# Performance work log

Measured on AMD Instinct MI355X. Metric: run time of the kernel, lower is better.

Reference implementation:

```python
import jax, jax.numpy as jnp
import numpy as np

EPS = 1e-12  # VERY_SMALL_NUMBER
LN_EPS = 1e-5
N, NFEAT, NHID, A, P, HOPS = 50000, 256, 128, 32, 4, 2


def setup_inputs() -> dict:
    key = jax.random.key(0)
    ks = jax.random.split(key, 16)
    def w(i, shape, scale=0.05):
        return jax.random.normal(ks[i], shape, dtype=jnp.float32) * scale
    return {
        "x": jax.random.normal(ks[0], (N, NFEAT), dtype=jnp.float32),
        # input_mapper: Linear(nfeat,nhid) -> ReLU -> Linear(nhid,nhid)
        "im_w1": w(1, (NFEAT, NHID)), "im_b1": jnp.zeros((NHID,), jnp.float32),
        "im_w2": w(2, (NHID, NHID)),  "im_b2": jnp.zeros((NHID,), jnp.float32),
        # AnchorGraphLearner
        "anchors": w(3, (A, NHID), 1.0),
        "ml_w1": w(4, (P, 2 * NHID, NHID)), "ml_b1": jnp.zeros((P, NHID), jnp.float32),
        "ml_w2": w(5, (P, NHID)),            "ml_b2": jnp.zeros((P,), jnp.float32),
        # AnchorGNNLayer weights (xavier in torch; scaled randn here)
        "enc_w": w(6, (HOPS, NHID, NHID)), "enc_b": jnp.zeros((HOPS, NHID), jnp.float32),
        # LayerNorm
        "ln_g": jnp.ones((NHID,), jnp.float32), "ln_b": jnp.zeros((NHID,), jnp.float32),
        # classifier: Linear -> PReLU(nhid) -> Linear(nhid,2)
        "cls_w1": w(7, (NHID, NHID)), "cls_b1": jnp.zeros((NHID,), jnp.float32),
        "prelu_a": jnp.full((NHID,), 0.25, jnp.float32),
        "cls_w2": w(8, (NHID, 2)),   "cls_b2": jnp.zeros((2,), jnp.float32),
    }


def _forward(x, im_w1, im_b1, im_w2, im_b2, anchors, ml_w1, ml_b1, ml_w2, ml_b2,
             enc_w, enc_b, ln_g, ln_b, cls_w1, cls_b1, prelu_a, cls_w2, cls_b2):
    nhid = im_w2.shape[-1]
    # input_mapper (dropout is identity in eval)
    h = jnp.maximum(x @ im_w1 + im_b1, 0.0) @ im_w2 + im_b2  # [N, nhid]
    x_loc = h

    # --- AnchorGraphLearner: fused form of cat([x_i, a_j]) @ W1 ---
    Wx, Wa = ml_w1[:, :nhid, :], ml_w1[:, nhid:, :]  # each [P, nhid, nhid]
    attn = jnp.zeros((h.shape[0], anchors.shape[0]), h.dtype)
    for p in range(ml_w1.shape[0]):  # small fixed head count
        hx = h @ Wx[p]                               # [N, nhid]
        ha = anchors @ Wa[p]                         # [A, nhid]
        hid = jnp.maximum(hx[:, None, :] + ha[None, :, :] + ml_b1[p], 0.0)  # [N, A, nhid]
        attn = attn + jax.nn.sigmoid(hid @ ml_w2[p] + ml_b2[p])            # [N, A]
    adj = attn / ml_w1.shape[0]  # mean over heads, [N, A]

    # --- AnchorGNNLayer stack (anchor_mp normalized double matmul) ---
    node_norm = adj / jnp.maximum(adj.sum(axis=0, keepdims=True), EPS)     # col-normalized [N, A]
    anchor_norm = adj / jnp.maximum(adj.sum(axis=1, keepdims=True), EPS)   # row-normalized [N, A]
    xc = h
    for i in range(enc_w.shape[0]):
        support = xc @ enc_w[i]                          # [N, nhid]
        agg = node_norm.T @ support                      # [A, nhid]
        xc = jnp.maximum(anchor_norm @ agg + enc_b[i], 0.0)

    # residual + LayerNorm
    z = xc + x_loc
    mu = z.mean(axis=-1, keepdims=True)
    var = ((z - mu) ** 2).mean(axis=-1, keepdims=True)
    z = (z - mu) * jax.lax.rsqrt(var + LN_EPS) * ln_g + ln_b

    def classifier(t):
        t1 = t @ cls_w1 + cls_b1
        t1 = jnp.where(t1 > 0, t1, prelu_a * t1)  # PReLU(nhid)
        return t1 @ cls_w2 + cls_b2

    pred = classifier(z)                 # [N, 2]
    anchor_logits = classifier(anchors)  # [A, 2]
    anchor_vec = anchors[None]           # [1, A, nhid] (matches unsqueeze(0))
    return (pred, z, anchor_vec, anchor_logits)


def reference(x, im_w1, im_b1, im_w2, im_b2, anchors, ml_w1, ml_b1, ml_w2, ml_b2,
              enc_w, enc_b, ln_g, ln_b, cls_w1, cls_b1, prelu_a, cls_w2, cls_b2):
    return _forward(x, im_w1, im_b1, im_w2, im_b2, anchors, ml_w1, ml_b1, ml_w2, ml_b2,
                    enc_w, enc_b, ln_g, ln_b, cls_w1, cls_b1, prelu_a, cls_w2, cls_b2)
```

## Files before the change

### kernel.cpp

```cpp
#include <hip/hip_runtime.h>
#include <math.h>

#define NN 50000
#define FEAT 256
#define HID 128
#define NA 32
#define NP 4
#define TM 64
#define NBLK 782
#define NB2 781
#define LDA 132
#define EPSS 1e-12f
#define LN_EPS 1e-5f

typedef unsigned short u16;
typedef __attribute__((ext_vector_type(8))) short bf16x8;
typedef __attribute__((ext_vector_type(4))) float f32x4;

#define ADJ_F   0
#define RS_F    1600000
#define CS_F    1650000
#define AGG0_F  1650032
#define AGG1_F  1654128
#define HB_F    1658256
#define FLAG_F  1674640
#define F_END   1674672
#define XC_U   (2 * F_END)
#define SUP_U  (XC_U + NN * HID)
#define PW_U   (SUP_U + NN * HID)
#define PW_TOT 165638
#define WS_NEED_BYTES ((size_t)(PW_U + PW_TOT) * 2ULL)
#define CSP_OFF 0

#define PK_IMW1T  0
#define PK_IMW2T  32768
#define PK_MLW1T  49152
#define PK_ENCWT  114688
#define PK_CLSW1T 147456
#define PK_IMB1   163840
#define PK_IMB2   163968
#define PK_MLW2   164096
#define PK_ENCB   164608
#define PK_LNG    164864
#define PK_LNB    164992
#define PK_CLSB1  165120
#define PK_PRELU  165248
#define PK_CLSW2  165376
#define PK_CLSB2  165632
#define PK_MLB2   165634
#define PK_TOTAL  165638

#define PRED_OFF 0
#define Z_OFF    100000
#define AV_OFF   6500000
#define AL_OFF   6504096
#define OUT_TOT  6504160

__device__ __constant__ int kNel[19] = {
    NN * FEAT, FEAT * HID, HID, HID * HID, HID, NA * HID,
    NP * 2 * HID * HID, NP * HID, NP * HID, NP, 2 * HID * HID, 2 * HID,
    HID, HID, HID * HID, HID, HID, HID * 2, 2};

#define TSEG_TOT 163840
__device__ __constant__ int tLen[9]  = {32768,16384,16384,16384,16384,16384,16384,16384,16384};
__device__ __constant__ int tDst[9]  = {PK_IMW1T,PK_IMW2T,PK_MLW1T,PK_MLW1T+16384,
                                        PK_MLW1T+32768,PK_MLW1T+49152,PK_ENCWT,
                                        PK_ENCWT+16384,PK_CLSW1T};
__device__ __constant__ int tSrcT[9] = {1,3,6,6,6,6,10,10,14};
__device__ __constant__ int tBase[9] = {0,0,0,32768,65536,98304,0,16384,0};
#define VSEG_TOT 1798
__device__ __constant__ int vLen[11] = {128,128,512,256,128,128,128,128,256,2,4};
__device__ __constant__ int vDst[11] = {PK_IMB1,PK_IMB2,PK_MLW2,PK_ENCB,PK_LNG,PK_LNB,
                                        PK_CLSB1,PK_PRELU,PK_CLSW2,PK_CLSB2,PK_MLB2};
__device__ __constant__ int vSrcT[11]= {2,4,8,11,12,13,15,16,17,18,9};

struct P19 { const void* q[19]; };

__device__ __forceinline__ float b2f(u16 u) {
    union { float f; unsigned int i; } v; v.i = ((unsigned int)u) << 16; return v.f;
}
__device__ __forceinline__ u16 f2b(float f) {
    union { float f; unsigned int i; } v; v.f = f;
    unsigned int x = v.i;
    x += 0x7fffu + ((x >> 16) & 1u);
    return (u16)(x >> 16);
}
__device__ __forceinline__ float ldf(const void* p, size_t i, int fl) {
    if (fl == 1) return ((const float*)p)[i];
    if (fl == 0) return b2f(((const u16*)p)[i]);
    return 0.f;
}

__global__ __launch_bounds__(256) void k_detect_all(P19 a, int* __restrict__ flags) {
    __shared__ int sHi[256], sE[256], sO[256];
    const int b = blockIdx.x;
    const u16* p = (const u16*)a.q[b];
    const int M = (kNel[b] < 8192) ? kNel[b] : 8192;
    int cHi = 0, cE = 0, cO = 0;
    for (int j = threadIdx.x; j < M; j += 256) {
        const u16 v = p[j];
        if (j & 1) cO += (v != 0);
        else { cE += (v != 0); cHi += (((v >> 7) & 0xFF) >= 200); }
    }
    sHi[threadIdx.x] = cHi; sE[threadIdx.x] = cE; sO[threadIdx.x] = cO;
    __syncthreads();
    for (int s = 128; s > 0; s >>= 1) {
        if (threadIdx.x < (unsigned)s) {
            sHi[threadIdx.x] += sHi[threadIdx.x + s];
            sE[threadIdx.x]  += sE[threadIdx.x + s];
            sO[threadIdx.x]  += sO[threadIdx.x + s];
        }
        __syncthreads();
    }
    if (threadIdx.x == 0) {
        int f;
        if (sE[0] == 0 && sO[0] == 0) f = 2;
        else if (sHi[0] >= 4 || sE[0] == 0) f = 1;
        else f = 0;
        flags[b] = f;
    }
}

__global__ __launch_bounds__(256) void k_convT(P19 a, const int* __restrict__ flags,
                                               u16* __restrict__ pw) {
    int idx = blockIdx.x * 256 + threadIdx.x;
    if (idx >= TSEG_TOT) return;
    int off = idx, s = 0;
    while (off >= tLen[s]) { off -= tLen[s]; ++s; }
    int n, k;
    if (s == 0) { n = off >> 8; k = off & 255; }
    else        { n = off >> 7; k = off & 127; }
    const int si = tSrcT[s];
    pw[tDst[s] + off] = f2b(ldf(a.q[si], (size_t)tBase[s] + (size_t)k * 128 + n,
                                flags[si]));
}

__global__ __launch_bounds__(256) void k_convV(P19 a, const int* __restrict__ flags,
                                               u16* __restrict__ pw) {
    for (int idx = threadIdx.x; idx < VSEG_TOT; idx += 256) {
        int off = idx, s = 0;
        while (off >= vLen[s]) { off -= vLen[s]; ++s; }
        const int si = vSrcT[s];
        pw[vDst[s] + off] = f2b(ldf(a.q[si], off, flags[si]));
    }
}

__device__ __forceinline__ void mfma_64x128(const u16* As, const u16* Bt,
                                            f32x4 acc[8], int lane, int rowBase) {
    const int lr = lane & 15, lq = lane >> 4;
#pragma unroll
    for (int kc = 0; kc < 4; ++kc) {
        bf16x8 a = *(const bf16x8*)(As + (rowBase + lr) * 136 + kc * 32 + lq * 8);
#pragma unroll
        for (int t = 0; t < 8; ++t) {
            bf16x8 b = *(const bf16x8*)(Bt + (t * 16 + lr) * 136 + kc * 32 + lq * 8);
            acc[t] = __builtin_amdgcn_mfma_f32_16x16x32_bf16(a, b, acc[t], 0, 0, 0);
        }
    }
}

template<int KTOT, int ACT, int AMODE, int OMODE>
__global__ __launch_bounds__(256) void k_gemm_m(const void* __restrict__ A,
                                                const u16* __restrict__ pw,
                                                void* __restrict__ outp,
                                                const int* __restrict__ flags,
                                                const int boff, const int biasOff) {
    __shared__ __align__(16) u16 As[64 * 136];
    __shared__ __align__(16) u16 Bt[128 * 136];
    const int fA = (AMODE == 0) ? flags[0] : 0;
    const int tid = threadIdx.x;
    const int row0 = blockIdx.x * TM;
    const int lane = tid & 63, wv = tid >> 6, rowBase = wv * 16;
    const int lr = lane & 15, lq = lane >> 4;
    f32x4 acc[8];
    const f32x4 z4 = {0.f, 0.f, 0.f, 0.f};
#pragma unroll
    for (int t = 0; t < 8; ++t) acc[t] = z4;

    for (int kc = 0; kc < KTOT / 128; ++kc) {
        for (int i = tid; i < 64 * 32; i += 256) {
            const int m = i >> 5, k4 = (i & 31) << 2;
            const int g = row0 + m;
            ushort4 o; o.x = 0; o.y = 0; o.z = 0; o.w = 0;
            if (g < NN) {
                const size_t idx = (size_t)g * KTOT + kc * 128 + k4;
                bool f32path = (AMODE == 2) || (AMODE == 0 && fA == 1);
                if (f32path) {
                    float4 v = *(const float4*)((const float*)A + idx);
                    o.x = f2b(v.x); o.y = f2b(v.y); o.z = f2b(v.z); o.w = f2b(v.w);
                } else {
                    o = *(const ushort4*)((const u16*)A + idx);
                }
            }
            *(ushort4*)&As[m * 136 + k4] = o;
        }
        for (int i = tid; i < 128 * 32; i += 256) {
            const int n = i >> 5, k4 = (i & 31) << 2;
            *(ushort4*)&Bt[n * 136 + k4] =
                *(const ushort4*)(pw + boff + (size_t)n * KTOT + kc * 128 + k4);
        }
        __syncthreads();
        mfma_64x128(As, Bt, acc, lane, rowBase);
        __syncthreads();
    }
#pragma unroll
    for (int t = 0; t < 8; ++t) {
        const int col = t * 16 + lr;
        const float bv = (biasOff >= 0) ? b2f(pw[biasOff + col]) : 0.f;
#pragma unroll
        for (int r = 0; r < 4; ++r) {
            const int g = row0 + rowBase + lq * 4 + r;
            if (g < NN) {
                float v = acc[t][r] + bv;
                if (ACT == 1) v = fmaxf(v, 0.f);
                if constexpr (OMODE == 0)
                    ((u16*)outp)[(size_t)g * HID + col] = f2b(v);
                else
                    ((float*)outp)[(size_t)g * HID + col] = v;
            }
        }
    }
}

__global__ __launch_bounds__(128) void k_pre(const void* __restrict__ anchors,
                                             const void* __restrict__ ml_w1,
                                             const void* __restrict__ ml_b1,
                                             float* __restrict__ hb,
                                             const int* __restrict__ flags) {
    __shared__ float sa[HID];
    const int fAn = flags[5], fW1 = flags[6], fB1 = flags[7];
    const int p = blockIdx.x >> 5, a = blockIdx.x & 31, k = threadIdx.x;
    sa[k] = ldf(anchors, a * HID + k, fAn);
    __syncthreads();
    float acc = ldf(ml_b1, p * HID + k, fB1);
    const size_t wbase = ((size_t)p * 2 * HID + HID) * HID + k;
#pragma unroll 4
    for (int j = 0; j < HID; ++j)
        acc += sa[j] * ldf(ml_w1, wbase + (size_t)j * HID, fW1);
    hb[p * (NA * HID) + k * NA + a] = acc;
}

__global__ __launch_bounds__(128) void k_wc(const float* __restrict__ hb,
                                            const u16* __restrict__ pw,
                                            float* __restrict__ wc) {
    __shared__ float red[128];
    const int p = blockIdx.x, tid = threadIdx.x;
    const int a = tid & 31, q = tid >> 5;
    float s = 0.f;
    for (int k = q * 32; k < q * 32 + 32; ++k)
        s += b2f(pw[PK_MLW2 + p * HID + k]) * hb[(size_t)p * (NA * HID) + k * NA + a];
    red[tid] = 0.5f * s;
    __syncthreads();
    if (tid < 32)
        wc[p * NA + tid] = red[tid] + red[tid + 32] + red[tid + 64] + red[tid + 96];
}

__global__ __launch_bounds__(256) void k_anchor(const void* __restrict__ anchors,
                                                const void* __restrict__ cls_w1,
                                                const void* __restrict__ cls_b1,
                                                const void* __restrict__ prelu_a,
                                                const void* __restrict__ cls_w2,
                                                const void* __restrict__ cls_b2,
                                                float* __restrict__ out,
                                                const int* __restrict__ flags) {
    __shared__ float sa[2][HID];
    __shared__ float st1[2][HID];
    const int fAn = flags[5], fW1 = flags[14], fB1 = flags[15];
    const int fPa = flags[16], fW2 = flags[17], fB2 = flags[18];
    const int tid = threadIdx.x;
    const int a0 = blockIdx.x * 2;
    const int half = tid >> 7, k = tid & 127;
    sa[half][k] = ldf(anchors, (a0 + half) * HID + k, fAn);
    __syncthreads();
    float acc = ldf(cls_b1, k, fB1);
#pragma unroll 4
    for (int j = 0; j < HID; ++j) acc += sa[half][j] * ldf(cls_w1, j * HID + k, fW1);
    const float pa = ldf(prelu_a, k, fPa);
    st1[half][k] = acc > 0.f ? acc : pa * acc;
    __syncthreads();
    if (tid < 4) {
        const int aa = tid >> 1, c = tid & 1;
        float s = ldf(cls_b2, c, fB2);
        for (int j = 0; j < HID; ++j) s += st1[aa][j] * ldf(cls_w2, j * 2 + c, fW2);
        out[AL_OFF + (a0 + aa) * 2 + c] = s;
    }
    if (blockIdx.x == 0) {
        for (int i = tid; i < NA * HID; i += 256)
            out[AV_OFF + i] = ldf(anchors, i, fAn);
    }
}

__global__ __launch_bounds__(256) void k_fattn(const float* __restrict__ h,
                                               const u16* __restrict__ pw,
                                               const float* __restrict__ hb,
                                               const float* __restrict__ wc,
                                               float* __restrict__ adj,
                                               float* __restrict__ rowsum,
                                               float* __restrict__ csPart) {
    __shared__ __align__(16) u16 Bt[128 * 136];
    __shared__ __align__(16) float hbs[128 * 32];
    __shared__ float hws[HID];
    __shared__ float wcs[NA];
    __shared__ float swr[4][NA];
    const int tid = threadIdx.x;
    const int row0 = blockIdx.x * TM;
    const int lane = tid & 63, wv = tid >> 6, rowBase = wv * 16;
    const int lr = lane & 15, lq = lane >> 4;
    const int g = tid & 3, myrow = tid >> 2;
    const int a0 = g * 8;

    bf16x8 afr[4];
    {
        const int gr = row0 + rowBase + lr;
#pragma unroll
        for (int kc = 0; kc < 4; ++kc) {
            bf16x8 t;
            if (gr < NN) {
                const float* src = h + (size_t)gr * HID + kc * 32 + lq * 8;
                float4 v0 = *(const float4*)src;
                float4 v1 = *(const float4*)(src + 4);
                t[0] = (short)f2b(v0.x); t[1] = (short)f2b(v0.y);
                t[2] = (short)f2b(v0.z); t[3] = (short)f2b(v0.w);
                t[4] = (short)f2b(v1.x); t[5] = (short)f2b(v1.y);
                t[6] = (short)f2b(v1.z); t[7] = (short)f2b(v1.w);
            } else {
#pragma unroll
                for (int j = 0; j < 8; ++j) t[j] = 0;
            }
            afr[kc] = t;
        }
    }

    float adjacc[8];
#pragma unroll
    for (int j = 0; j < 8; ++j) adjacc[j] = 0.f;

    for (int p = 0; p < NP; ++p) {
        __syncthreads();
        for (int i = tid; i < 128 * 32; i += 256) {
            const int n = i >> 5, k4 = (i & 31) << 2;
            *(ushort4*)&Bt[n * 136 + k4] =
                *(const ushort4*)(pw + PK_MLW1T + p * 16384 + n * 128 + k4);
        }
        const float* hbp = hb + (size_t)p * (NA * HID);
        for (int i = tid; i < 1024; i += 256)
            *(float4*)&hbs[i * 4] = *(const float4*)(hbp + i * 4);
        if (tid < HID) hws[tid] = 0.5f * b2f(pw[PK_MLW2 + p * HID + tid]);
        if (tid < NA) wcs[tid] = wc[p * NA + tid];
        __syncthreads();

        f32x4 acc[8];
        const f32x4 z4 = {0.f, 0.f, 0.f, 0.f};
#pragma unroll
        for (int t = 0; t < 8; ++t) acc[t] = z4;
#pragma unroll
        for (int kc = 0; kc < 4; ++kc)
#pragma unroll
            for (int t = 0; t < 8; ++t) {
                bf16x8 b = *(const bf16x8*)(Bt + (t * 16 + lr) * 136 + kc * 32 + lq * 8);
                acc[t] = __builtin_amdgcn_mfma_f32_16x16x32_bf16(afr[kc], b, acc[t], 0, 0, 0);
            }
        __syncthreads();
#pragma unroll
        for (int t = 0; t < 8; ++t)
#pragma unroll
            for (int r = 0; r < 4; ++r)
                Bt[(rowBase + lq * 4 + r) * 136 + t * 16 + lr] = f2b(acc[t][r]);
        __syncthreads();

        const float b2v = b2f(pw[PK_MLB2 + p]);
        float sabs[8], wh = 0.f;
#pragma unroll
        for (int j = 0; j < 8; ++j) sabs[j] = 0.f;

#pragma unroll 4
        for (int kp = 0; kp < 64; ++kp) {
            const unsigned hx2 = *(const unsigned*)&Bt[myrow * 136 + kp * 2];
            union { unsigned u; float f; } u0, u1;
            u0.u = hx2 << 16;
            u1.u = hx2 & 0xffff0000u;
            const float f0 = u0.f, f1 = u1.f;
            const float2 hw2 = *(const float2*)&hws[kp * 2];
            wh = fmaf(hw2.x, f0, wh);
            wh = fmaf(hw2.y, f1, wh);
            const float4 c00 = *(const float4*)&hbs[(kp * 2) * NA + a0];
            const float4 c01 = *(const float4*)&hbs[(kp * 2) * NA + a0 + 4];
            const float4 c10 = *(const float4*)&hbs[(kp * 2 + 1) * NA + a0];
            const float4 c11 = *(const float4*)&hbs[(kp * 2 + 1) * NA + a0 + 4];
            sabs[0] = fmaf(hw2.x, fabsf(f0 + c00.x), sabs[0]);
            sabs[1] = fmaf(hw2.x, fabsf(f0 + c00.y), sabs[1]);
            sabs[2] = fmaf(hw2.x, fabsf(f0 + c00.z), sabs[2]);
            sabs[3] = fmaf(hw2.x, fabsf(f0 + c00.w), sabs[3]);
            sabs[4] = fmaf(hw2.x, fabsf(f0 + c01.x), sabs[4]);
            sabs[5] = fmaf(hw2.x, fabsf(f0 + c01.y), sabs[5]);
            sabs[6] = fmaf(hw2.x, fabsf(f0 + c01.z), sabs[6]);
            sabs[7] = fmaf(hw2.x, fabsf(f0 + c01.w), sabs[7]);
            sabs[0] = fmaf(hw2.y, fabsf(f1 + c10.x), sabs[0]);
            sabs[1] = fmaf(hw2.y, fabsf(f1 + c10.y), sabs[1]);
            sabs[2] = fmaf(hw2.y, fabsf(f1 + c10.z), sabs[2]);
            sabs[3] = fmaf(hw2.y, fabsf(f1 + c10.w), sabs[3]);
            sabs[4] = fmaf(hw2.y, fabsf(f1 + c11.x), sabs[4]);
            sabs[5] = fmaf(hw2.y, fabsf(f1 + c11.y), sabs[5]);
            sabs[6] = fmaf(hw2.y, fabsf(f1 + c11.z), sabs[6]);
            sabs[7] = fmaf(hw2.y, fabsf(f1 + c11.w), sabs[7]);
        }
#pragma unroll
        for (int j = 0; j < 8; ++j) {
            const float s = wh + wcs[a0 + j] + b2v + sabs[j];
            adjacc[j] += 0.25f / (1.f + __expf(-s));
        }
    }

    const int grow = row0 + myrow;
    if (grow >= NN) {
#pragma unroll
        for (int j = 0; j < 8; ++j) adjacc[j] = 0.f;
    }
    if (grow < NN) {
        float* dst = adj + (size_t)grow * NA + a0;
        *(float4*)dst = make_float4(adjacc[0], adjacc[1], adjacc[2], adjacc[3]);
        *(float4*)(dst + 4) = make_float4(adjacc[4], adjacc[5], adjacc[6], adjacc[7]);
    }
    float rs = 0.f;
#pragma unroll
    for (int j = 0; j < 8; ++j) rs += adjacc[j];
    rs += __shfl_xor(rs, 1);
    rs += __shfl_xor(rs, 2);
    if (g == 0 && grow < NN) rowsum[grow] = rs;
#pragma unroll
    for (int st = 4; st <= 32; st <<= 1)
#pragma unroll
        for (int j = 0; j < 8; ++j) adjacc[j] += __shfl_xor(adjacc[j], st);
    if (lane < 4) {
#pragma unroll
        for (int j = 0; j < 8; ++j) swr[wv][lane * 8 + j] = adjacc[j];
    }
    __syncthreads();
    if (tid < NA)
        csPart[tid * NBLK + blockIdx.x] =
            swr[0][tid] + swr[1][tid] + swr[2][tid] + swr[3][tid];
}

__global__ __launch_bounds__(256) void k_cs_red(const float* __restrict__ csPart,
                                                float* __restrict__ colsum) {
    __shared__ float red[256];
    const int a = blockIdx.x, tid = threadIdx.x;
    float s = 0.f;
    for (int b = tid; b < NBLK; b += 256) s += csPart[a * NBLK + b];
    red[tid] = s;
    __syncthreads();
    for (int st = 128; st > 0; st >>= 1) {
        if (tid < st) red[tid] += red[tid + st];
        __syncthreads();
    }
    if (tid == 0) colsum[a] = red[0];
}

__global__ __launch_bounds__(256) void k_aggT(const float* __restrict__ adj,
                                              const float* __restrict__ h,
                                              float* __restrict__ part) {
    __shared__ float sT[TM][LDA];
    __shared__ float adjT[TM][NA + 1];
    const int tid = threadIdx.x;
    const int a0 = (tid & 15) * 2, k0 = (tid >> 4) * 8;
    float acc[2][8];
#pragma unroll
    for (int ia = 0; ia < 2; ++ia)
#pragma unroll
        for (int j = 0; j < 8; ++j) acc[ia][j] = 0.f;

    const int nt = (blockIdx.x == NB2 - 1) ? 2 : 1;
    for (int t = 0; t < nt; ++t) {
        const int row0 = (blockIdx.x + t) * TM;
        __syncthreads();
        for (int i = tid; i < TM * 32; i += 256) {
            const int m = i >> 5, k4 = (i & 31) << 2, g = row0 + m;
            float4 v = make_float4(0.f, 0.f, 0.f, 0.f);
            if (g < NN) v = *(const float4*)(h + (size_t)g * HID + k4);
            *(float4*)&sT[m][k4] = v;
        }
        for (int i = tid; i < TM * NA; i += 256) {
            const int m = i >> 5, a = i & 31, g = row0 + m;
            adjT[m][a] = (g < NN) ? adj[(size_t)g * NA + a] : 0.f;
        }
        __syncthreads();
#pragma unroll 4
        for (int n = 0; n < TM; ++n) {
            const float a0v = adjT[n][a0], a1v = adjT[n][a0 + 1];
            float4 s0 = *(const float4*)&sT[n][k0];
            float4 s1 = *(const float4*)&sT[n][k0 + 4];
            float sv[8] = {s0.x, s0.y, s0.z, s0.w, s1.x, s1.y, s1.z, s1.w};
#pragma unroll
            for (int j = 0; j < 8; ++j) {
                acc[0][j] += a0v * sv[j];
                acc[1][j] += a1v * sv[j];
            }
        }
    }
    float* dst = part + (size_t)blockIdx.x * (NA * HID);
#pragma unroll
    for (int ia = 0; ia < 2; ++ia) {
        *(float4*)&dst[(a0 + ia) * HID + k0] =
            make_float4(acc[ia][0], acc[ia][1], acc[ia][2], acc[ia][3]);
        *(float4*)&dst[(a0 + ia) * HID + k0 + 4] =
            make_float4(acc[ia][4], acc[ia][5], acc[ia][6], acc[ia][7]);
    }
}

__global__ __launch_bounds__(256) void k_Tred(const float* __restrict__ part,
                                              float* __restrict__ T) {
    __shared__ float red[256];
    const int jj = threadIdx.x & 15, bq = threadIdx.x >> 4;
    const int j = blockIdx.x * 16 + jj;
    float s = 0.f;
#pragma unroll 8
    for (int b = bq; b < NB2; b += 16) s += part[(size_t)b * (NA * HID) + j];
    red[threadIdx.x] = s;
    __syncthreads();
    if (bq == 0) {
        float t = 0.f;
#pragma unroll
        for (int q = 0; q < 16; ++q) t += red[q * 16 + jj];
        T[j] = t;
    }
}

__global__ __launch_bounds__(128) void k_small(const float* __restrict__ T,
                                               const u16* __restrict__ pw,
                                               const int hop,
                                               float* __restrict__ agg) {
    __shared__ float tr[HID];
    const int a = blockIdx.x, n = threadIdx.x;
    tr[n] = T[a * HID + n];
    __syncthreads();
    const u16* w = pw + PK_ENCWT + hop * HID * HID + n * HID;
    float s = 0.f;
#pragma unroll 4
    for (int j4 = 0; j4 < HID; j4 += 4) {
        ushort4 u = *(const ushort4*)(w + j4);
        s += tr[j4] * b2f(u.x) + tr[j4 + 1] * b2f(u.y) +
             tr[j4 + 2] * b2f(u.z) + tr[j4 + 3] * b2f(u.w);
    }
    agg[a * HID + n] = s;
}

__global__ __launch_bounds__(256) void k_e2a(const float* __restrict__ adj,
                                             const float* __restrict__ rowsum,
                                             const float* __restrict__ colsum,
                                             const float* __restrict__ agg,
                                             const u16* __restrict__ pw,
                                             float* __restrict__ part) {
    __shared__ float aggn[NA][LDA];
    __shared__ float adjT[TM][NA + 1];
    __shared__ __align__(8) u16 xcs[TM * 136];
    __shared__ float csl[NA], rsl[TM];
    const int tid = threadIdx.x;
    const int n0 = (tid & 31) * 4, m0 = (tid >> 5) * 8;
    const int a0 = (tid & 15) * 2, k0 = (tid >> 4) * 8;

    if (tid < NA) csl[tid] = fmaxf(colsum[tid], EPSS);
    __syncthreads();
    for (int i = tid; i < (NA * HID) / 4; i += 256) {
        const int a = i >> 5, k4 = (i & 31) << 2;
        float4 v = *(const float4*)(agg + a * HID + k4);
        const float inv = 1.f / csl[a];
        v.x *= inv; v.y *= inv; v.z *= inv; v.w *= inv;
        *(float4*)&aggn[a][k4] = v;
    }
    float bv[4];
#pragma unroll
    for (int j = 0; j < 4; ++j) bv[j] = b2f(pw[PK_ENCB + n0 + j]);

    float acc2[2][8];
#pragma unroll
    for (int ia = 0; ia < 2; ++ia)
#pragma unroll
        for (int j = 0; j < 8; ++j) acc2[ia][j] = 0.f;

    const int nt = (blockIdx.x == NB2 - 1) ? 2 : 1;
    for (int t = 0; t < nt; ++t) {
        const int row0 = (blockIdx.x + t) * TM;
        __syncthreads();
        for (int i = tid; i < TM * NA; i += 256) {
            const int m = i >> 5, a = i & 31, g = row0 + m;
            adjT[m][a] = (g < NN) ? adj[(size_t)g * NA + a] : 0.f;
        }
        if (tid >= 64 && tid < 128) {
            const int m = tid - 64, g = row0 + m;
            rsl[m] = (g < NN) ? 1.f / fmaxf(rowsum[g], EPSS) : 0.f;
        }
        __syncthreads();
        float acc[8][4];
#pragma unroll
        for (int i = 0; i < 8; ++i)
#pragma unroll
            for (int j = 0; j < 4; ++j) acc[i][j] = 0.f;
        for (int a = 0; a < NA; ++a) {
            float4 gv = *(const float4*)&aggn[a][n0];
            float gvv[4] = {gv.x, gv.y, gv.z, gv.w};
#pragma unroll
            for (int i = 0; i < 8; ++i) {
                const float av = adjT[m0 + i][a];
#pragma unroll
                for (int j = 0; j < 4; ++j) acc[i][j] += av * gvv[j];
            }
        }
#pragma unroll
        for (int i = 0; i < 8; ++i) {
            const float r = rsl[m0 + i];
            ushort4 o;
            o.x = f2b(fmaxf(r * acc[i][0] + bv[0], 0.f));
            o.y = f2b(fmaxf(r * acc[i][1] + bv[1], 0.f));
            o.z = f2b(fmaxf(r * acc[i][2] + bv[2], 0.f));
            o.w = f2b(fmaxf(r * acc[i][3] + bv[3], 0.f));
            *(ushort4*)&xcs[(m0 + i) * 136 + n0] = o;
        }
        __syncthreads();
#pragma unroll 4
        for (int n = 0; n < TM; ++n) {
            const float a0v = adjT[n][a0], a1v = adjT[n][a0 + 1];
            ushort4 u0 = *(const ushort4*)&xcs[n * 136 + k0];
            ushort4 u1 = *(const ushort4*)&xcs[n * 136 + k0 + 4];
            float sv[8] = {b2f(u0.x), b2f(u0.y), b2f(u0.z), b2f(u0.w),
                           b2f(u1.x), b2f(u1.y), b2f(u1.z), b2f(u1.w)};
#pragma unroll
            for (int j = 0; j < 8; ++j) {
                acc2[0][j] += a0v * sv[j];
                acc2[1][j] += a1v * sv[j];
            }
        }
    }
    float* dst = part + (size_t)blockIdx.x * (NA * HID);
#pragma unroll
    for (int ia = 0; ia < 2; ++ia) {
        *(float4*)&dst[(a0 + ia) * HID + k0] =
            make_float4(acc2[ia][0], acc2[ia][1], acc2[ia][2], acc2[ia][3]);
        *(float4*)&dst[(a0 + ia) * HID + k0 + 4] =
            make_float4(acc2[ia][4], acc2[ia][5], acc2[ia][6], acc2[ia][7]);
    }
}

__global__ __launch_bounds__(256) void k_e2f(const float* __restrict__ adj,
                                             const float* __restrict__ rowsum,
                                             const float* __restrict__ colsum,
                                             const float* __restrict__ agg,
                                             const u16* __restrict__ pw,
                                             float* __restrict__ out) {
    __shared__ __align__(16) u16 As[64 * 136];
    __shared__ __align__(16) u16 uniB[128 * 136];
    __shared__ float smu[TM], sinv[TM], sg[HID], sb[HID], w2s[2 * HID];
    __shared__ float csl[NA], rsl[TM];
    float* aggn  = (float*)As;
    float* adjTf = (float*)uniB;
    float* zT    = (float*)uniB;
    const int tid = threadIdx.x;
    const int row0 = blockIdx.x * TM;
    const int lane = tid & 63, wv = tid >> 6, rowBase = wv * 16;
    const int lr = lane & 15, lq = lane >> 4;
    const int n0 = (tid & 31) * 4, m0 = (tid >> 5) * 8;
    const float* h = out + Z_OFF;

    if (tid < NA) csl[tid] = fmaxf(colsum[tid], EPSS);
    if (tid >= 64 && tid < 128) {
        const int m = tid - 64, g = row0 + m;
        rsl[m] = (g < NN) ? 1.f / fmaxf(rowsum[g], EPSS) : 0.f;
    }
    for (int i = tid; i < TM * NA; i += 256) {
        const int m = i >> 5, a = i & 31, g = row0 + m;
        adjTf[m * (NA + 1) + a] = (g < NN) ? adj[(size_t)g * NA + a] : 0.f;
    }
    __syncthreads();
    for (int i = tid; i < (NA * HID) / 4; i += 256) {
        const int a = i >> 5, k4 = (i & 31) << 2;
        float4 v = *(const float4*)(agg + a * HID + k4);
        const float inv = 1.f / csl[a];
        v.x *= inv; v.y *= inv; v.z *= inv; v.w *= inv;
        *(float4*)&aggn[a * LDA + k4] = v;
    }
    __syncthreads();
    float acc[8][4];
#pragma unroll
    for (int i = 0; i < 8; ++i)
#pragma unroll
        for (int j = 0; j < 4; ++j) acc[i][j] = 0.f;
    for (int a = 0; a < NA; ++a) {
        float4 gv = *(const float4*)&aggn[a * LDA + n0];
        float gvv[4] = {gv.x, gv.y, gv.z, gv.w};
#pragma unroll
        for (int i = 0; i < 8; ++i) {
            const float av = adjTf[(m0 + i) * (NA + 1) + a];
#pragma unroll
            for (int j = 0; j < 4; ++j) acc[i][j] += av * gvv[j];
        }
    }
    float bv[4];
#pragma unroll
    for (int j = 0; j < 4; ++j) bv[j] = b2f(pw[PK_ENCB + HID + n0 + j]);
    float xcv[8][4];
#pragma unroll
    for (int i = 0; i < 8; ++i) {
        const float r = rsl[m0 + i];
#pragma unroll
        for (int j = 0; j < 4; ++j)
            xcv[i][j] = fmaxf(r * acc[i][j] + bv[j], 0.f);
    }
    __syncthreads();
#pragma unroll
    for (int i = 0; i < 8; ++i) {
        const int g = row0 + m0 + i;
        float4 hv = make_float4(0.f, 0.f, 0.f, 0.f);
        if (g < NN) hv = *(const float4*)(h + (size_t)g * HID + n0);
        float4 zv = make_float4(xcv[i][0] + hv.x, xcv[i][1] + hv.y,
                                xcv[i][2] + hv.z, xcv[i][3] + hv.w);
        *(float4*)&zT[(m0 + i) * 132 + n0] = zv;
    }
    if (tid < HID) { sg[tid] = b2f(pw[PK_LNG + tid]); sb[tid] = b2f(pw[PK_LNB + tid]); }
    w2s[tid] = b2f(pw[PK_CLSW2 + tid]);
    __syncthreads();
    if (tid < TM) {
        float s = 0.f;
        for (int k = 0; k < HID; ++k) s += zT[tid * 132 + k];
        const float mu = s * (1.f / HID);
        float v = 0.f;
        for (int k = 0; k < HID; ++k) { const float d = zT[tid * 132 + k] - mu; v += d * d; }
        smu[tid] = mu;
        sinv[tid] = rsqrtf(v * (1.f / HID) + LN_EPS);
    }
    __syncthreads();
    for (int i = tid; i < TM * 32; i += 256) {
        const int m = i >> 5, k4 = (i & 31) << 2, g = row0 + m;
        float4 v = *(const float4*)&zT[m * 132 + k4];
        const float mu = smu[m], inv = sinv[m];
        v.x = (v.x - mu) * inv * sg[k4 + 0] + sb[k4 + 0];
        v.y = (v.y - mu) * inv * sg[k4 + 1] + sb[k4 + 1];
        v.z = (v.z - mu) * inv * sg[k4 + 2] + sb[k4 + 2];
        v.w = (v.w - mu) * inv * sg[k4 + 3] + sb[k4 + 3];
        if (g < NN) *(float4*)&out[Z_OFF + (size_t)g * HID + k4] = v;
        ushort4 o; o.x = f2b(v.x); o.y = f2b(v.y); o.z = f2b(v.z); o.w = f2b(v.w);
        *(ushort4*)&As[m * 136 + k4] = o;
    }
    __syncthreads();
    for (int i = tid; i < 128 * 32; i += 256) {
        const int n = i >> 5, k4 = (i & 31) << 2;
        *(ushort4*)&uniB[n * 136 + k4] =
            *(const ushort4*)(pw + PK_CLSW1T + n * 128 + k4);
    }
    __syncthreads();
    f32x4 macc[8];
    const f32x4 z4 = {0.f, 0.f, 0.f, 0.f};
#pragma unroll
    for (int t = 0; t < 8; ++t) macc[t] = z4;
    mfma_64x128(As, uniB, macc, lane, rowBase);
    __syncthreads();
#pragma unroll
    for (int t = 0; t < 8; ++t) {
        const int col = t * 16 + lr;
        const float bc = b2f(pw[PK_CLSB1 + col]);
        const float pa = b2f(pw[PK_PRELU + col]);
#pragma unroll
        for (int r = 0; r < 4; ++r) {
            float v = macc[t][r] + bc;
            v = v > 0.f ? v : pa * v;
            As[(rowBase + lq * 4 + r) * 136 + col] = f2b(v);
        }
    }
    __syncthreads();
    if (tid < 128) {
        const int r = tid >> 1, c = tid & 1, g = row0 + r;
        if (g < NN) {
            float s = b2f(pw[PK_CLSB2 + c]);
            for (int k = 0; k < HID; ++k) s += b2f(As[r * 136 + k]) * w2s[k * 2 + c];
            out[PRED_OFF + (size_t)g * 2 + c] = s;
        }
    }
}

extern "C" void kernel_launch(void* const* d_in, const int* in_sizes, int n_in,
                              void* d_out, int out_size, void* d_ws, size_t ws_size,
                              hipStream_t stream) {
    const bool ok = (n_in >= 19) && (out_size == OUT_TOT) &&
                    (ws_size >= WS_NEED_BYTES) &&
                    (in_sizes[0] == NN * FEAT) && (in_sizes[6] == NP * 2 * HID * HID) &&
                    (in_sizes[10] == 2 * HID * HID) && (in_sizes[17] == HID * 2);
    if (!ok) {
        hipMemsetAsync(d_out, 0, (size_t)OUT_TOT * 4, stream);
        return;
    }

    float* ws    = (float*)d_ws;
    u16*   wsu   = (u16*)d_ws;
    float* out   = (float*)d_out;
    int*   flags = (int*)(ws + FLAG_F);
    float* hbuf  = out + Z_OFF;
    u16*   supb  = wsu + SUP_U;
    u16*   pw    = wsu + PW_U;
    float* xcf   = (float*)(wsu + XC_U);
    float* csPart = xcf + CSP_OFF;
    float* partb = (float*)(wsu + SUP_U);
    float* Tbuf  = ws + HB_F;
    float* wcv   = ws + AGG1_F;

    P19 pa;
    for (int i = 0; i < 19; ++i) pa.q[i] = d_in[i];
    k_detect_all<<<19, 256, 0, stream>>>(pa, flags);
    k_convT<<<(TSEG_TOT + 255) / 256, 256, 0, stream>>>(pa, flags, pw);
    k_convV<<<1, 256, 0, stream>>>(pa, flags, pw);

    k_pre<<<NP * NA, 128, 0, stream>>>(d_in[5], d_in[6], d_in[7], ws + HB_F, flags);
    k_wc<<<NP, 128, 0, stream>>>(ws + HB_F, pw, wcv);
    k_anchor<<<NA / 2, 256, 0, stream>>>(d_in[5], d_in[14], d_in[15], d_in[16],
                                         d_in[17], d_in[18], out, flags);

    k_gemm_m<FEAT, 1, 0, 0><<<NBLK, 256, 0, stream>>>(d_in[0], pw, supb, flags,
                                                      PK_IMW1T, PK_IMB1);
    k_gemm_m<HID, 0, 1, 1><<<NBLK, 256, 0, stream>>>(supb, pw, hbuf, flags,
                                                     PK_IMW2T, PK_IMB2);

    k_fattn<<<NBLK, 256, 0, stream>>>(hbuf, pw, ws + HB_F, wcv, ws + ADJ_F,
                                      ws + RS_F, csPart);
    k_cs_red<<<NA, 256, 0, stream>>>(csPart, ws + CS_F);

    k_aggT<<<NB2, 256, 0, stream>>>(ws + ADJ_F, hbuf, partb);
    k_Tred<<<256, 256, 0, stream>>>(partb, Tbuf);
    k_small<<<NA, 128, 0, stream>>>(Tbuf, pw, 0, ws + AGG0_F);
    k_e2a<<<NB2, 256, 0, stream>>>(ws + ADJ_F, ws + RS_F, ws + CS_F, ws + AGG0_F,
                                   pw, partb);
    k_Tred<<<256, 256, 0, stream>>>(partb, Tbuf);
    k_small<<<NA, 128, 0, stream>>>(Tbuf, pw, 1, ws + AGG1_F);
    k_e2f<<<NBLK, 256, 0, stream>>>(ws + ADJ_F, ws + RS_F, ws + CS_F, ws + AGG1_F,
                                    pw, out);
}
```

Baseline: 469.9 us.

## Fuse input-mapper GEMMs into one kernel and alias attention LDS buffers

Merges the two input-mapper GEMMs into one kernel. The ReLU'd first-layer tile stays in LDS as bf16 and is fed straight into the second GEMM, removing the intermediate global write and read and one launch. In the attention kernel, the anchor-bias table is staged through registers and written into the unused half of the B-tile LDS buffer after the MFMA phase, cutting LDS footprint to allow higher occupancy. Global loads of the table are issued before the GEMM to overlap latency, at the cost of extra registers.

```diff
diff --git a/kernel.cpp b/kernel.cpp
--- a/kernel.cpp
+++ b/kernel.cpp
@@ -159,15 +159,13 @@
     }
 }
 
-template<int KTOT, int ACT, int AMODE, int OMODE>
-__global__ __launch_bounds__(256) void k_gemm_m(const void* __restrict__ A,
-                                                const u16* __restrict__ pw,
-                                                void* __restrict__ outp,
-                                                const int* __restrict__ flags,
-                                                const int boff, const int biasOff) {
+__global__ __launch_bounds__(256) void k_gemm2(const void* __restrict__ A,
+                                               const u16* __restrict__ pw,
+                                               float* __restrict__ outh,
+                                               const int* __restrict__ flags) {
     __shared__ __align__(16) u16 As[64 * 136];
     __shared__ __align__(16) u16 Bt[128 * 136];
-    const int fA = (AMODE == 0) ? flags[0] : 0;
+    const int fA = flags[0];
     const int tid = threadIdx.x;
     const int row0 = blockIdx.x * TM;
     const int lane = tid & 63, wv = tid >> 6, rowBase = wv * 16;
@@ -177,15 +175,14 @@
 #pragma unroll
     for (int t = 0; t < 8; ++t) acc[t] = z4;
 
-    for (int kc = 0; kc < KTOT / 128; ++kc) {
+    for (int kc = 0; kc < 2; ++kc) {
         for (int i = tid; i < 64 * 32; i += 256) {
             const int m = i >> 5, k4 = (i & 31) << 2;
             const int g = row0 + m;
             ushort4 o; o.x = 0; o.y = 0; o.z = 0; o.w = 0;
             if (g < NN) {
-                const size_t idx = (size_t)g * KTOT + kc * 128 + k4;
-                bool f32path = (AMODE == 2) || (AMODE == 0 && fA == 1);
-                if (f32path) {
+                const size_t idx = (size_t)g * FEAT + kc * 128 + k4;
+                if (fA == 1) {
                     float4 v = *(const float4*)((const float*)A + idx);
                     o.x = f2b(v.x); o.y = f2b(v.y); o.z = f2b(v.z); o.w = f2b(v.w);
                 } else {
@@ -197,7 +194,7 @@
         for (int i = tid; i < 128 * 32; i += 256) {
             const int n = i >> 5, k4 = (i & 31) << 2;
             *(ushort4*)&Bt[n * 136 + k4] =
-                *(const ushort4*)(pw + boff + (size_t)n * KTOT + kc * 128 + k4);
+                *(const ushort4*)(pw + PK_IMW1T + (size_t)n * FEAT + kc * 128 + k4);
         }
         __syncthreads();
         mfma_64x128(As, Bt, acc, lane, rowBase);
@@ -206,18 +203,29 @@
 #pragma unroll
     for (int t = 0; t < 8; ++t) {
         const int col = t * 16 + lr;
-        const float bv = (biasOff >= 0) ? b2f(pw[biasOff + col]) : 0.f;
+        const float bv = b2f(pw[PK_IMB1 + col]);
+#pragma unroll
+        for (int r = 0; r < 4; ++r)
+            As[(rowBase + lq * 4 + r) * 136 + col] = f2b(fmaxf(acc[t][r] + bv, 0.f));
+    }
+    for (int i = tid; i < 128 * 32; i += 256) {
+        const int n = i >> 5, k4 = (i & 31) << 2;
+        *(ushort4*)&Bt[n * 136 + k4] =
+            *(const ushort4*)(pw + PK_IMW2T + (size_t)n * HID + k4);
+    }
+    __syncthreads();
+    f32x4 acc2[8];
+#pragma unroll
+    for (int t = 0; t < 8; ++t) acc2[t] = z4;
+    mfma_64x128(As, Bt, acc2, lane, rowBase);
+#pragma unroll
+    for (int t = 0; t < 8; ++t) {
+        const int col = t * 16 + lr;
+        const float bv = b2f(pw[PK_IMB2 + col]);
 #pragma unroll
         for (int r = 0; r < 4; ++r) {
             const int g = row0 + rowBase + lq * 4 + r;
-            if (g < NN) {
-                float v = acc[t][r] + bv;
-                if (ACT == 1) v = fmaxf(v, 0.f);
-                if constexpr (OMODE == 0)
-                    ((u16*)outp)[(size_t)g * HID + col] = f2b(v);
-                else
-                    ((float*)outp)[(size_t)g * HID + col] = v;
-            }
+            if (g < NN) outh[(size_t)g * HID + col] = acc2[t][r] + bv;
         }
     }
 }
@@ -298,10 +306,10 @@
                                                float* __restrict__ rowsum,
                                                float* __restrict__ csPart) {
     __shared__ __align__(16) u16 Bt[128 * 136];
-    __shared__ __align__(16) float hbs[128 * 32];
     __shared__ float hws[HID];
     __shared__ float wcs[NA];
     __shared__ float swr[4][NA];
+    float* hbf = (float*)&Bt[64 * 136];
     const int tid = threadIdx.x;
     const int row0 = blockIdx.x * TM;
     const int lane = tid & 63, wv = tid >> 6, rowBase = wv * 16;
@@ -342,9 +350,12 @@
             *(ushort4*)&Bt[n * 136 + k4] =
                 *(const ushort4*)(pw + PK_MLW1T + p * 16384 + n * 128 + k4);
         }
-        const float* hbp = hb + (size_t)p * (NA * HID);
-        for (int i = tid; i < 1024; i += 256)
-            *(float4*)&hbs[i * 4] = *(const float4*)(hbp + i * 4);
+        float4 hbreg[4];
+        {
+            const float4* hbp4 = (const float4*)(hb + (size_t)p * (NA * HID));
+#pragma unroll
+            for (int j = 0; j < 4; ++j) hbreg[j] = hbp4[tid + j * 256];
+        }
         if (tid < HID) hws[tid] = 0.5f * b2f(pw[PK_MLW2 + p * HID + tid]);
         if (tid < NA) wcs[tid] = wc[p * NA + tid];
         __syncthreads();
@@ -366,6 +377,9 @@
 #pragma unroll
             for (int r = 0; r < 4; ++r)
                 Bt[(rowBase + lq * 4 + r) * 136 + t * 16 + lr] = f2b(acc[t][r]);
+#pragma unroll
+        for (int j = 0; j < 4; ++j)
+            ((float4*)hbf)[tid + j * 256] = hbreg[j];
         __syncthreads();
 
         const float b2v = b2f(pw[PK_MLB2 + p]);
@@ -383,10 +397,10 @@
             const float2 hw2 = *(const float2*)&hws[kp * 2];
             wh = fmaf(hw2.x, f0, wh);
             wh = fmaf(hw2.y, f1, wh);
-            const float4 c00 = *(const float4*)&hbs[(kp * 2) * NA + a0];
-            const float4 c01 = *(const float4*)&hbs[(kp * 2) * NA + a0 + 4];
-            const float4 c10 = *(const float4*)&hbs[(kp * 2 + 1) * NA + a0];
-            const float4 c11 = *(const float4*)&hbs[(kp * 2 + 1) * NA + a0 + 4];
+            const float4 c00 = *(const float4*)&hbf[(kp * 2) * NA + a0];
+            const float4 c01 = *(const float4*)&hbf[(kp * 2) * NA + a0 + 4];
+            const float4 c10 = *(const float4*)&hbf[(kp * 2 + 1) * NA + a0];
+            const float4 c11 = *(const float4*)&hbf[(kp * 2 + 1) * NA + a0 + 4];
             sabs[0] = fmaf(hw2.x, fabsf(f0 + c00.x), sabs[0]);
             sabs[1] = fmaf(hw2.x, fabsf(f0 + c00.y), sabs[1]);
             sabs[2] = fmaf(hw2.x, fabsf(f0 + c00.z), sabs[2]);
@@ -792,7 +806,6 @@
     float* out   = (float*)d_out;
     int*   flags = (int*)(ws + FLAG_F);
     float* hbuf  = out + Z_OFF;
-    u16*   supb  = wsu + SUP_U;
     u16*   pw    = wsu + PW_U;
     float* xcf   = (float*)(wsu + XC_U);
     float* csPart = xcf + CSP_OFF;
@@ -811,10 +824,7 @@
     k_anchor<<<NA / 2, 256, 0, stream>>>(d_in[5], d_in[14], d_in[15], d_in[16],
                                          d_in[17], d_in[18], out, flags);
 
-    k_gemm_m<FEAT, 1, 0, 0><<<NBLK, 256, 0, stream>>>(d_in[0], pw, supb, flags,
-                                                      PK_IMW1T, PK_IMB1);
-    k_gemm_m<HID, 0, 1, 1><<<NBLK, 256, 0, stream>>>(supb, pw, hbuf, flags,
-                                                     PK_IMW2T, PK_IMB2);
+    k_gemm2<<<NBLK, 256, 0, stream>>>(d_in[0], pw, hbuf, flags);
 
     k_fattn<<<NBLK, 256, 0, stream>>>(hbuf, pw, ws + HB_F, wcv, ws + ADJ_F,
                                       ws + RS_F, csPart);
```

After: 446.4 us. -5.0%, faster.
